# Optimization experiments

Hardware: AMD Instinct MI355X
Metric: run time of the kernel (lower is better)

Reference implementation:

```python
import jax, jax.numpy as jnp
import numpy as np
from jax import lax

EPS = 1e-5

def _conv(x, w, b):
    # sign-binarized conv: sign(x) conv sign(w) + float bias; 3x3, pad 1, NCHW
    y = lax.conv_general_dilated(jnp.sign(x), jnp.sign(w), (1, 1), ((1, 1), (1, 1)),
                                 dimension_numbers=("NCHW", "OIHW", "NCHW"))
    return y + b[None, :, None, None]

def _bn(x, g, beta, mean, var):
    # eval-mode batchnorm with running stats
    inv = g / jnp.sqrt(var + EPS)
    return x * inv[None, :, None, None] + (beta - mean * inv)[None, :, None, None]

def _pool2(x):
    return lax.reduce_window(x, -jnp.inf, lax.max, (1, 1, 2, 2), (1, 1, 2, 2), "VALID")

def setup_inputs() -> dict:
    key = jax.random.key(0)
    ks = jax.random.split(key, 16)
    B, num_classes = 4096, 2
    x = jax.random.normal(ks[0], (B, 1, 64, 64), dtype=jnp.float32)
    def conv_params(k, cout, cin):
        k1, k2 = jax.random.split(k)
        w = jax.random.normal(k1, (cout, cin, 3, 3), dtype=jnp.float32) * 0.1
        b = jax.random.normal(k2, (cout,), dtype=jnp.float32) * 0.01
        return w, b
    def bn_params(k, c):
        k1, k2, k3 = jax.random.split(k, 3)
        g = 1.0 + 0.1 * jax.random.normal(k1, (c,), dtype=jnp.float32)
        beta = 0.1 * jax.random.normal(k2, (c,), dtype=jnp.float32)
        mean = 0.1 * jax.random.normal(k3, (c,), dtype=jnp.float32)
        var = jnp.ones((c,), dtype=jnp.float32)
        return g, beta, mean, var
    w1, b1 = conv_params(ks[1], 8, 1)
    w2, b2 = conv_params(ks[2], 16, 8)
    w3, b3 = conv_params(ks[3], 32, 16)
    g1, be1, m1, v1 = bn_params(ks[4], 8)
    g2, be2, m2, v2 = bn_params(ks[5], 16)
    g3, be3, m3, v3 = bn_params(ks[6], 32)
    fc_w = jax.random.normal(ks[7], (num_classes, 32 * 8 * 8), dtype=jnp.float32) * 0.02
    fc_b = jnp.zeros((num_classes,), dtype=jnp.float32)
    return dict(x=x, w1=w1, b1=b1, g1=g1, be1=be1, m1=m1, v1=v1,
                w2=w2, b2=b2, g2=g2, be2=be2, m2=m2, v2=v2,
                w3=w3, b3=b3, g3=g3, be3=be3, m3=m3, v3=v3,
                fc_w=fc_w, fc_b=fc_b)

def reference(x, w1, b1, g1, be1, m1, v1,
              w2, b2, g2, be2, m2, v2,
              w3, b3, g3, be3, m3, v3, fc_w, fc_b):
    h = _pool2(jax.nn.relu(_bn(_conv(x, w1, b1), g1, be1, m1, v1)))   # [B,8,32,32]
    h = _pool2(jax.nn.relu(_bn(_conv(h, w2, b2), g2, be2, m2, v2)))   # [B,16,16,16]
    h = _pool2(jax.nn.relu(_bn(_conv(h, w3, b3), g3, be3, m3, v3)))   # [B,32,8,8]
    h = h.reshape(h.shape[0], -1)                                      # [B,2048]
    logits = h @ fc_w.T + fc_b
    return jax.nn.softmax(logits, axis=1)
```

## Files before the change

### kernel.cpp

```cpp
#include <hip/hip_runtime.h>
#include <stdint.h>

#define EPS 1e-5f
typedef unsigned long long u64;
typedef unsigned int u32;
typedef unsigned short u16;
typedef unsigned char u8;

struct Consts {
  u32 p2r[16][4];
  u64 q3m0[32];
  u64 q3m1[32];
  u32 q3m2[32];
  int lo2[16];
  u32 rng2[16];
  float inv3[32];
  float A3[32];
  float b3v[32];
  float fcb[2];
  u8  lut[9 * 512];
};
static_assert(sizeof(Consts) == 6024, "layout");

__global__ void prep_kernel(
    const float* __restrict__ w1, const float* __restrict__ b1,
    const float* __restrict__ g1, const float* __restrict__ be1,
    const float* __restrict__ m1, const float* __restrict__ v1,
    const float* __restrict__ w2, const float* __restrict__ b2,
    const float* __restrict__ g2, const float* __restrict__ be2,
    const float* __restrict__ m2, const float* __restrict__ v2,
    const float* __restrict__ w3, const float* __restrict__ b3,
    const float* __restrict__ g3, const float* __restrict__ be3,
    const float* __restrict__ m3, const float* __restrict__ v3,
    const float* __restrict__ fcb, Consts* __restrict__ out)
{
  int tid = threadIdx.x;

  if (blockIdx.x == 0) {
    if (tid < 16) {
      int c = tid;
      u32 rm[3] = {0u, 0u, 0u};
      for (int ci = 0; ci < 8; ++ci)
        for (int t = 0; t < 9; ++t) {
          float w = w2[(c * 8 + ci) * 9 + t];
          if (w > 0.f) rm[t / 3] |= 1u << ((t % 3) * 8 + ci);
        }
      out->p2r[c][0] = rm[0]; out->p2r[c][1] = rm[1];
      out->p2r[c][2] = rm[2]; out->p2r[c][3] = 0u;
      float inv = __fdiv_rn(g2[c], __fsqrt_rn(__fadd_rn(v2[c], EPS)));
      float A   = __fsub_rn(be2[c], __fmul_rn(m2[c], inv));
      int lo = 1000, hi = -1000;
      for (int s = -72; s <= 72; ++s) {
        float y  = __fadd_rn((float)s, b2[c]);
        float bn = __fadd_rn(__fmul_rn(y, inv), A);
        if (bn > 0.f) { if (s < lo) lo = s; if (s > hi) hi = s; }
      }
      out->lo2[c] = lo; out->rng2[c] = (u32)(hi - lo);
    }
    if (tid < 32) {
      int c = tid;
      u64 q0 = 0, q1 = 0; u32 q2 = 0;
      for (int ci = 0; ci < 16; ++ci)
        for (int t = 0; t < 9; ++t) {
          float w = w3[(c * 16 + ci) * 9 + t];
          if (w > 0.f) {
            if (t < 4)      q0 |= 1ull << (t * 16 + ci);
            else if (t < 8) q1 |= 1ull << ((t - 4) * 16 + ci);
            else            q2 |= 1u << ci;
          }
        }
      out->q3m0[c] = q0; out->q3m1[c] = q1; out->q3m2[c] = q2;
      float inv = __fdiv_rn(g3[c], __fsqrt_rn(__fadd_rn(v3[c], EPS)));
      out->inv3[c] = inv;
      out->A3[c]   = __fsub_rn(be3[c], __fmul_rn(m3[c], inv));
      out->b3v[c]  = b3[c];
    }
    if (tid < 2) out->fcb[tid] = fcb[tid];
    return;
  }

  __shared__ float inv1s[8], A1s[8];
  __shared__ int   sw1[8][9];
  if (tid < 8) {
    int c = tid;
    float inv = __fdiv_rn(g1[c], __fsqrt_rn(__fadd_rn(v1[c], EPS)));
    inv1s[c] = inv;
    A1s[c]   = __fsub_rn(be1[c], __fmul_rn(m1[c], inv));
    for (int t = 0; t < 9; ++t) sw1[c][t] = (w1[c * 9 + t] > 0.f) ? 1 : -1;
  }
  __syncthreads();
  int e = (blockIdx.x - 1) * 256 + tid;
  int type = e >> 9, pat = e & 511;
  int ty = type / 3, tx = type % 3;
  u8 byte = 0;
  for (int c = 0; c < 8; ++c) {
    int s = 0;
    for (int t = 0; t < 9; ++t) {
      int dr = t / 3, dc = t % 3;
      bool valid = !((ty == 0 && dr == 0) || (ty == 2 && dr == 2) ||
                     (tx == 0 && dc == 0) || (tx == 2 && dc == 2));
      if (!valid) continue;
      s += ((pat >> t) & 1) ? sw1[c][t] : -sw1[c][t];
    }
    float y  = __fadd_rn((float)s, b1[c]);
    float bn = __fadd_rn(__fmul_rn(y, inv1s[c]), A1s[c]);
    if (bn > 0.f) byte |= (u8)(1u << c);
  }
  out->lut[e] = byte;
}

__device__ __forceinline__ void pair_sync(u32* flag, int lane, u32 target) {
  __threadfence_block();
  if (lane == 0) atomicAdd(flag, 1u);
  while (*(volatile u32*)flag < target) __builtin_amdgcn_s_sleep(2);
  __threadfence_block();
}

__launch_bounds__(256, 4)
__global__ void main_kernel(const float* __restrict__ x, const float* __restrict__ fcw,
                            const Consts* __restrict__ cs, float* __restrict__ out, int B)
{
  __shared__ __align__(16) u8  slut[9 * 512];
  __shared__ __align__(16) u64 xb[2][64];
  __shared__ __align__(16) u8  s2p[2][34][36];
  __shared__ __align__(16) u16 s3p[2][18][18];
  __shared__ float red[2][2][2];
  __shared__ u32 bar[2];

  const int tid = threadIdx.x;
  const int wv = tid >> 6, lane = tid & 63;
  const int im = wv >> 1, w = wv & 1;
  const int img = blockIdx.x * 2 + im;

  for (int i = tid; i < 1152; i += 256) ((u32*)slut)[i] = ((const u32*)cs->lut)[i];
  for (int i = tid; i < 612; i += 256) ((u32*)s2p)[i] = 0;
  for (int i = tid; i < 324; i += 256) ((u32*)s3p)[i] = 0;
  if (tid < 2) bar[tid] = 0u;
  __syncthreads();

  if (img < B) {
    const float* xp = x + (size_t)img * 4096 + (size_t)w * 2048;
    u64 my = 0;
    #pragma unroll 4
    for (int rr = 0; rr < 32; ++rr) {
      float v = xp[rr * 64 + lane];
      u64 m = __ballot(v > 0.f);
      if (lane == rr) my = m;
    }
    if (lane < 32) xb[im][w * 32 + lane] = my;
  }
  pair_sync(&bar[im], lane, 2u);

  {
    const int c = lane & 31, h = lane >> 5;
    const int j0 = 2 * c;
    const u32 sa0  = (c == 0) ? 0u : (u32)(j0 - 1);
    const u32 msk0 = (c == 0) ? 3u : 7u;
    const u32 sft0 = (c == 0) ? 1u : 0u;
    const u32 base0 = ((c == 0) ? 0u : 1u) << 9;
    const u32 base1 = ((c == 31) ? 2u : 1u) << 9;
    #pragma unroll
    for (int p = 0; p < 8; ++p) {
      const int pr = w * 16 + h * 8 + p;
      const int i0 = 2 * pr;
      u64 r0 = (i0 > 0) ? xb[im][i0 - 1] : 0ull;
      u64 r1 = xb[im][i0];
      u64 r2 = xb[im][i0 + 1];
      u64 r3 = (i0 + 2 < 64) ? xb[im][i0 + 2] : 0ull;
      u32 acc = 0;
      #pragma unroll
      for (int a = 0; a < 2; ++a) {
        u64 ra = a ? r1 : r0, rb = a ? r2 : r1, rc = a ? r3 : r2;
        const int i = i0 + a;
        const u32 ti9 = ((i == 0) ? 0u : ((i == 63) ? 6u : 3u)) << 9;
        u32 ea = ((u32)(ra >> sa0) & msk0) << sft0;
        u32 eb = ((u32)(rb >> sa0) & msk0) << sft0;
        u32 ec = ((u32)(rc >> sa0) & msk0) << sft0;
        acc |= slut[ti9 + base0 + (ea | (eb << 3) | (ec << 6))];
        u32 fa = (u32)(ra >> j0) & 7u;
        u32 fb = (u32)(rb >> j0) & 7u;
        u32 fc = (u32)(rc >> j0) & 7u;
        acc |= slut[ti9 + base1 + (fa | (fb << 3) | (fc << 6))];
      }
      s2p[im][pr + 1][c + 1] = (u8)acc;
    }
  }
  pair_sync(&bar[im], lane, 4u);

  {
    const int idx = w * 64 + lane;
    const int pi = idx >> 3, pjp = idx & 7;
    const int bo = 4 * pjp;
    const u32* rp0 = (const u32*)&s2p[im][2 * pi + 0][bo];
    const u32* rp1 = (const u32*)&s2p[im][2 * pi + 1][bo];
    const u32* rp2 = (const u32*)&s2p[im][2 * pi + 2][bo];
    const u32* rp3 = (const u32*)&s2p[im][2 * pi + 3][bo];
    u32 rl[4], rh[4];
    rl[0] = rp0[0]; rh[0] = rp0[1];
    rl[1] = rp1[0]; rh[1] = rp1[1];
    rl[2] = rp2[0]; rh[2] = rp2[1];
    rl[3] = rp3[0]; rh[3] = rp3[1];

    u32 d0[8], d1[8], d2[8]; int pc[8]; u32 cw[8];
    #pragma unroll
    for (int k = 0; k < 8; ++k) {
      const int o = k >> 2, a = (k >> 1) & 1, bb = k & 1;
      const int sh = 8 * (2 * o + bb);
      d0[k] = __builtin_amdgcn_alignbit(rh[a],     rl[a],     sh) & 0xFFFFFFu;
      d1[k] = __builtin_amdgcn_alignbit(rh[a + 1], rl[a + 1], sh) & 0xFFFFFFu;
      d2[k] = __builtin_amdgcn_alignbit(rh[a + 2], rl[a + 2], sh) & 0xFFFFFFu;
      pc[k] = __popc(d0[k]) + __popc(d1[k]) + __popc(d2[k]);
      cw[k] = 0u;
    }

    #pragma unroll 1
    for (int ch = 15; ch >= 0; --ch) {
      const u32 m0 = cs->p2r[ch][0];
      const u32 m1 = cs->p2r[ch][1];
      const u32 m2 = cs->p2r[ch][2];
      const int nlo = -cs->lo2[ch];
      const u32 rng = cs->rng2[ch];
      #pragma unroll
      for (int k = 0; k < 8; ++k) {
        int ps = __popc(d0[k] & m0) + __popc(d1[k] & m1) + __popc(d2[k] & m2);
        u32 t = (u32)(2 * ps - pc[k] + nlo);
        cw[k] = cw[k] + cw[k] + ((t <= rng) ? 1u : 0u);
      }
    }
    s3p[im][pi + 1][2 * pjp + 1] = (u16)(cw[0] | cw[1] | cw[2] | cw[3]);
    s3p[im][pi + 1][2 * pjp + 2] = (u16)(cw[4] | cw[5] | cw[6] | cw[7]);
  }
  pair_sync(&bar[im], lane, 6u);

  float l0 = 0.f, l1 = 0.f;
  {
    const int pi = lane >> 3, pj = lane & 7;
    const u32* p0 = (const u32*)(&s3p[im][2 * pi + 0][2 * pj]);
    const u32* p1 = (const u32*)(&s3p[im][2 * pi + 1][2 * pj]);
    const u32* p2 = (const u32*)(&s3p[im][2 * pi + 2][2 * pj]);
    const u32* p3 = (const u32*)(&s3p[im][2 * pi + 3][2 * pj]);
    const u64 rr0 = (u64)p0[0] | ((u64)p0[1] << 32);
    const u64 rr1 = (u64)p1[0] | ((u64)p1[1] << 32);
    const u64 rr2 = (u64)p2[0] | ((u64)p2[1] << 32);
    const u64 rr3 = (u64)p3[0] | ((u64)p3[1] << 32);

    u64 q0a, q1a, q0b, q1b, q0c, q1c, q0d, q1d;
    u32 q2a, q2b, q2c, q2d;
    int pca, pcb, pcc, pcd;
    {
      u64 ta, tb, tc;
      ta = rr0;       tb = rr1;       tc = rr2;
      q0a = (ta & 0xFFFFFFFFFFFFull) | ((tb & 0xFFFFull) << 48);
      q1a = ((tb >> 16) & 0xFFFFFFFFull) | ((tc & 0xFFFFFFFFull) << 32);
      q2a = (u32)((tc >> 32) & 0xFFFFull);
      pca = __popcll(q0a) + __popcll(q1a) + __popc(q2a);
      ta = rr0 >> 16; tb = rr1 >> 16; tc = rr2 >> 16;
      q0b = (ta & 0xFFFFFFFFFFFFull) | ((tb & 0xFFFFull) << 48);
      q1b = ((tb >> 16) & 0xFFFFFFFFull) | ((tc & 0xFFFFFFFFull) << 32);
      q2b = (u32)((tc >> 32) & 0xFFFFull);
      pcb = __popcll(q0b) + __popcll(q1b) + __popc(q2b);
      ta = rr1;       tb = rr2;       tc = rr3;
      q0c = (ta & 0xFFFFFFFFFFFFull) | ((tb & 0xFFFFull) << 48);
      q1c = ((tb >> 16) & 0xFFFFFFFFull) | ((tc & 0xFFFFFFFFull) << 32);
      q2c = (u32)((tc >> 32) & 0xFFFFull);
      pcc = __popcll(q0c) + __popcll(q1c) + __popc(q2c);
      ta = rr1 >> 16; tb = rr2 >> 16; tc = rr3 >> 16;
      q0d = (ta & 0xFFFFFFFFFFFFull) | ((tb & 0xFFFFull) << 48);
      q1d = ((tb >> 16) & 0xFFFFFFFFull) | ((tc & 0xFFFFFFFFull) << 32);
      q2d = (u32)((tc >> 32) & 0xFFFFull);
      pcd = __popcll(q0d) + __popcll(q1d) + __popc(q2d);
    }

    #pragma unroll 2
    for (int cc = 0; cc < 16; ++cc) {
      const int c = 16 * w + cc;
      const u64 m0 = cs->q3m0[c], m1 = cs->q3m1[c];
      const u32 m2 = cs->q3m2[c];
      int t0 = 2 * (__popcll(q0a & m0) + __popcll(q1a & m1) + __popc(q2a & m2)) - pca;
      int t1 = 2 * (__popcll(q0b & m0) + __popcll(q1b & m1) + __popc(q2b & m2)) - pcb;
      int t2 = 2 * (__popcll(q0c & m0) + __popcll(q1c & m1) + __popc(q2c & m2)) - pcc;
      int t3 = 2 * (__popcll(q0d & m0) + __popcll(q1d & m1) + __popc(q2d & m2)) - pcd;
      int smax = max(max(t0, t1), max(t2, t3));
      int smin = min(min(t0, t1), min(t2, t3));
      float inv = cs->inv3[c];
      int sel = (inv > 0.f) ? smax : smin;
      float y   = __fadd_rn((float)sel, cs->b3v[c]);
      float bn  = __fadd_rn(__fmul_rn(y, inv), cs->A3[c]);
      float val = fmaxf(bn, 0.f);
      const int f = (c << 6) + lane;
      l0 = fmaf(val, fcw[f], l0);
      l1 = fmaf(val, fcw[2048 + f], l1);
    }
  }

  #pragma unroll
  for (int d = 32; d >= 1; d >>= 1) {
    l0 += __shfl_xor(l0, d, 64);
    l1 += __shfl_xor(l1, d, 64);
  }
  if (lane == 0) { red[im][w][0] = l0; red[im][w][1] = l1; }
  pair_sync(&bar[im], lane, 8u);
  if (w == 0 && lane == 0 && img < B) {
    float a0 = red[im][0][0] + red[im][1][0] + cs->fcb[0];
    float a1 = red[im][0][1] + red[im][1][1] + cs->fcb[1];
    float mm = fmaxf(a0, a1);
    float e0 = expf(a0 - mm), e1 = expf(a1 - mm);
    float sden = e0 + e1;
    out[(size_t)img * 2]     = e0 / sden;
    out[(size_t)img * 2 + 1] = e1 / sden;
  }
}

extern "C" void kernel_launch(void* const* d_in, const int* in_sizes, int n_in,
                              void* d_out, int out_size, void* d_ws, size_t ws_size,
                              hipStream_t stream) {
  const float* x   = (const float*)d_in[0];
  const float* w1  = (const float*)d_in[1];
  const float* b1  = (const float*)d_in[2];
  const float* g1  = (const float*)d_in[3];
  const float* be1 = (const float*)d_in[4];
  const float* m1  = (const float*)d_in[5];
  const float* v1  = (const float*)d_in[6];
  const float* w2  = (const float*)d_in[7];
  const float* b2  = (const float*)d_in[8];
  const float* g2  = (const float*)d_in[9];
  const float* be2 = (const float*)d_in[10];
  const float* m2  = (const float*)d_in[11];
  const float* v2  = (const float*)d_in[12];
  const float* w3  = (const float*)d_in[13];
  const float* b3  = (const float*)d_in[14];
  const float* g3  = (const float*)d_in[15];
  const float* be3 = (const float*)d_in[16];
  const float* m3  = (const float*)d_in[17];
  const float* v3  = (const float*)d_in[18];
  const float* fcw = (const float*)d_in[19];
  const float* fcb = (const float*)d_in[20];

  int B = in_sizes[0] / 4096;
  Consts* cs = (Consts*)d_ws;

  prep_kernel<<<19, 256, 0, stream>>>(w1, b1, g1, be1, m1, v1,
                                      w2, b2, g2, be2, m2, v2,
                                      w3, b3, g3, be3, m3, v3, fcb, cs);
  int nblk = (B + 1) / 2;
  main_kernel<<<nblk, 256, 0, stream>>>(x, fcw, cs, (float*)d_out, B);
}
```

Measured before the change: 67.55 us.

## Replace per-image spin barriers with block syncs and prefetch inputs and FC weights

Swaps the atomic-counter spin-wait pair barriers for plain __syncthreads across the whole block, removing the atomics and sleep polling. It also issues all 32 row loads of the input image up front before the ballots, and preloads this wave's FC weights into registers before the conv2 stage so their global latency overlaps the compute. In exchange, the two images in a block now wait for each other at every stage, and the extra live registers could pressure occupancy under the 256x4 launch bound.

```diff
diff --git a/kernel.cpp b/kernel.cpp
--- a/kernel.cpp
+++ b/kernel.cpp
@@ -109,13 +109,6 @@
   out->lut[e] = byte;
 }
 
-__device__ __forceinline__ void pair_sync(u32* flag, int lane, u32 target) {
-  __threadfence_block();
-  if (lane == 0) atomicAdd(flag, 1u);
-  while (*(volatile u32*)flag < target) __builtin_amdgcn_s_sleep(2);
-  __threadfence_block();
-}
-
 __launch_bounds__(256, 4)
 __global__ void main_kernel(const float* __restrict__ x, const float* __restrict__ fcw,
                             const Consts* __restrict__ cs, float* __restrict__ out, int B)
@@ -125,7 +118,6 @@
   __shared__ __align__(16) u8  s2p[2][34][36];
   __shared__ __align__(16) u16 s3p[2][18][18];
   __shared__ float red[2][2][2];
-  __shared__ u32 bar[2];
 
   const int tid = threadIdx.x;
   const int wv = tid >> 6, lane = tid & 63;
@@ -135,21 +127,21 @@
   for (int i = tid; i < 1152; i += 256) ((u32*)slut)[i] = ((const u32*)cs->lut)[i];
   for (int i = tid; i < 612; i += 256) ((u32*)s2p)[i] = 0;
   for (int i = tid; i < 324; i += 256) ((u32*)s3p)[i] = 0;
-  if (tid < 2) bar[tid] = 0u;
-  __syncthreads();
 
   if (img < B) {
     const float* xp = x + (size_t)img * 4096 + (size_t)w * 2048;
+    float xv[32];
+    #pragma unroll
+    for (int rr = 0; rr < 32; ++rr) xv[rr] = xp[rr * 64 + lane];
     u64 my = 0;
-    #pragma unroll 4
+    #pragma unroll
     for (int rr = 0; rr < 32; ++rr) {
-      float v = xp[rr * 64 + lane];
-      u64 m = __ballot(v > 0.f);
+      u64 m = __ballot(xv[rr] > 0.f);
       if (lane == rr) my = m;
     }
     if (lane < 32) xb[im][w * 32 + lane] = my;
   }
-  pair_sync(&bar[im], lane, 2u);
+  __syncthreads();
 
   {
     const int c = lane & 31, h = lane >> 5;
@@ -185,7 +177,15 @@
       s2p[im][pr + 1][c + 1] = (u8)acc;
     }
   }
-  pair_sync(&bar[im], lane, 4u);
+  __syncthreads();
+
+  float fw0[16], fw1[16];
+  #pragma unroll
+  for (int cc = 0; cc < 16; ++cc) {
+    const int f = ((16 * w + cc) << 6) + lane;
+    fw0[cc] = fcw[f];
+    fw1[cc] = fcw[2048 + f];
+  }
 
   {
     const int idx = w * 64 + lane;
@@ -230,7 +230,7 @@
     s3p[im][pi + 1][2 * pjp + 1] = (u16)(cw[0] | cw[1] | cw[2] | cw[3]);
     s3p[im][pi + 1][2 * pjp + 2] = (u16)(cw[4] | cw[5] | cw[6] | cw[7]);
   }
-  pair_sync(&bar[im], lane, 6u);
+  __syncthreads();
 
   float l0 = 0.f, l1 = 0.f;
   {
@@ -287,9 +287,8 @@
       float y   = __fadd_rn((float)sel, cs->b3v[c]);
       float bn  = __fadd_rn(__fmul_rn(y, inv), cs->A3[c]);
       float val = fmaxf(bn, 0.f);
-      const int f = (c << 6) + lane;
-      l0 = fmaf(val, fcw[f], l0);
-      l1 = fmaf(val, fcw[2048 + f], l1);
+      l0 = fmaf(val, fw0[cc], l0);
+      l1 = fmaf(val, fw1[cc], l1);
     }
   }
 
@@ -299,8 +298,8 @@
     l1 += __shfl_xor(l1, d, 64);
   }
   if (lane == 0) { red[im][w][0] = l0; red[im][w][1] = l1; }
-  pair_sync(&bar[im], lane, 8u);
-  if (w == 0 && lane == 0 && img < B) {
+  __syncthreads();
+  if ((tid & 127) == 0 && img < B) {
     float a0 = red[im][0][0] + red[im][1][0] + cs->fcb[0];
     float a1 = red[im][0][1] + red[im][1][1] + cs->fcb[1];
     float mm = fmaxf(a0, a1);
```

After: 65.23 us. -3.4%, faster.
